# Kernel optimization log

Measured on AMD Instinct MI355X. Metric: run time of the kernel, lower is better.

## Reference

```python
import jax, jax.numpy as jnp
import numpy as np

B = 4096  # number of rows (batch of 1-D sequences)
N = 4096  # transform length


def setup_inputs() -> dict:
    key = jax.random.key(0)
    x = jax.random.normal(key, (B, N), dtype=jnp.float32)
    # get_expk(N): expk[k] = (cos(pi*k/(2N)), -sin(pi*k/(2N)))
    t = jnp.arange(N, dtype=jnp.float32) * (np.pi / (2.0 * N))
    expk = jnp.stack([jnp.cos(t), -jnp.sin(t)], axis=-1)  # [N, 2]
    return {"x": x, "expk": expk}


def reference(x, expk):
    # IDCT (DCT-III), 2N-point FFT formulation:
    #   y_k = x_0 + 2 * sum_{n=1}^{N-1} x_n cos(pi*n*(2k+1)/(2N))
    #       = Re{ sum_n w_n x_n exp(j*pi*n/(2N)) * exp(j*2*pi*n*k/(2N)) },  w_0=1, w_n=2
    # i.e. the first N outputs of a 2N-point inverse DFT of the zero-padded,
    # twiddle-premultiplied sequence.
    n = x.shape[-1]
    # expk stores (cos(theta), -sin(theta)) => exp(+j*theta) = expk0 - j*expk1
    coef = (expk[..., 0] - 1j * expk[..., 1]).astype(jnp.complex64)  # [N]
    w = jnp.concatenate([jnp.ones((1,), x.dtype), jnp.full((n - 1,), 2.0, x.dtype)])
    a = (x * w).astype(jnp.complex64) * coef                      # [B, N]
    A = jnp.concatenate([a, jnp.zeros_like(a)], axis=-1)          # [B, 2N] zero-pad
    y = jnp.real(jnp.fft.ifft(A, axis=-1))[..., :n] * (2.0 * n)   # undo 1/(2N) of ifft
    return y.astype(x.dtype)
```

## Files before the change

### kernel.cpp

```cpp
#include <hip/hip_runtime.h>


#define NROW 4096
#define M    2048
#define NT   128
#define SWZ2(a) ((a) ^ ((((a) >> 4) & 7) << 1))

__device__ __forceinline__ void cmul(float ar, float ai, float br, float bi,
                                     float& orr, float& oii) {
    orr = ar * br - ai * bi;
    oii = ar * bi + ai * br;
}

__device__ __forceinline__ void dft16(float vr[16], float vi[16]) {
    constexpr float WR[4][4] = {
        {1.f, 1.f, 1.f, 1.f},
        {1.f,  0.92387953251128674f,  0.70710678118654752f,  0.38268343236508977f},
        {1.f,  0.70710678118654752f,  0.f,                  -0.70710678118654752f},
        {1.f,  0.38268343236508977f, -0.70710678118654752f, -0.92387953251128674f}};
    constexpr float WI[4][4] = {
        {0.f, 0.f, 0.f, 0.f},
        {0.f,  0.38268343236508977f,  0.70710678118654752f,  0.92387953251128674f},
        {0.f,  0.70710678118654752f,  1.f,                   0.70710678118654752f},
        {0.f,  0.92387953251128674f,  0.70710678118654752f, -0.38268343236508977f}};
    float ur[16], ui[16];
#pragma unroll
    for (int p = 0; p < 4; ++p) {
        float apcr = vr[p] + vr[p + 8],      apci = vi[p] + vi[p + 8];
        float amcr = vr[p] - vr[p + 8],      amci = vi[p] - vi[p + 8];
        float bpdr = vr[p + 4] + vr[p + 12], bpdi = vi[p + 4] + vi[p + 12];
        float bmdr = vr[p + 4] - vr[p + 12], bmdi = vi[p + 4] - vi[p + 12];
        float y0r = apcr + bpdr, y0i = apci + bpdi;
        float y1r = amcr - bmdi, y1i = amci + bmdr;
        float y2r = apcr - bpdr, y2i = apci - bpdi;
        float y3r = amcr + bmdi, y3i = amci - bmdr;
        ur[4 * p + 0] = y0r;  ui[4 * p + 0] = y0i;
        cmul(y1r, y1i, WR[p][1], WI[p][1], ur[4 * p + 1], ui[4 * p + 1]);
        cmul(y2r, y2i, WR[p][2], WI[p][2], ur[4 * p + 2], ui[4 * p + 2]);
        cmul(y3r, y3i, WR[p][3], WI[p][3], ur[4 * p + 3], ui[4 * p + 3]);
    }
#pragma unroll
    for (int q = 0; q < 4; ++q) {
        float apcr = ur[q] + ur[q + 8],      apci = ui[q] + ui[q + 8];
        float amcr = ur[q] - ur[q + 8],      amci = ui[q] - ui[q + 8];
        float bpdr = ur[q + 4] + ur[q + 12], bpdi = ui[q + 4] + ui[q + 12];
        float bmdr = ur[q + 4] - ur[q + 12], bmdi = ui[q + 4] - ui[q + 12];
        vr[q]      = apcr + bpdr;  vi[q]      = apci + bpdi;
        vr[q + 4]  = amcr - bmdi;  vi[q + 4]  = amci + bmdr;
        vr[q + 8]  = apcr - bpdr;  vi[q + 8]  = apci - bpdi;
        vr[q + 12] = amcr + bmdi;  vi[q + 12] = amci - bmdr;
    }
}

__device__ __forceinline__ void dft4(float& ar, float& ai, float& br, float& bi,
                                     float& cr, float& ci, float& dr, float& di) {
    float s02r = ar + cr, s02i = ai + ci;
    float d02r = ar - cr, d02i = ai - ci;
    float s13r = br + dr, s13i = bi + di;
    float d13r = br - dr, d13i = bi - di;
    ar = s02r + s13r; ai = s02i + s13i;
    br = d02r - d13i; bi = d02i + d13r;
    cr = s02r - s13r; ci = s02i - s13i;
    dr = d02r + d13i; di = d02i - d13r;
}

__device__ __forceinline__ void dft8(float* vr, float* vi) {
    float er[4]  = {vr[0], vr[2], vr[4], vr[6]};
    float ei[4]  = {vi[0], vi[2], vi[4], vi[6]};
    float odr[4] = {vr[1], vr[3], vr[5], vr[7]};
    float odi[4] = {vi[1], vi[3], vi[5], vi[7]};
    dft4(er[0], ei[0], er[1], ei[1], er[2], ei[2], er[3], ei[3]);
    dft4(odr[0], odi[0], odr[1], odi[1], odr[2], odi[2], odr[3], odi[3]);
    const float s = 0.70710678118654752f;
    vr[0] = er[0] + odr[0];            vi[0] = ei[0] + odi[0];
    vr[4] = er[0] - odr[0];            vi[4] = ei[0] - odi[0];
    float t1r = s * (odr[1] - odi[1]), t1i = s * (odr[1] + odi[1]);
    vr[1] = er[1] + t1r;               vi[1] = ei[1] + t1i;
    vr[5] = er[1] - t1r;               vi[5] = ei[1] - t1i;
    vr[2] = er[2] - odi[2];            vi[2] = ei[2] + odr[2];
    vr[6] = er[2] + odi[2];            vi[6] = ei[2] - odr[2];
    float t3r = -s * (odr[3] + odi[3]), t3i = s * (odr[3] - odi[3]);
    vr[3] = er[3] + t3r;               vi[3] = ei[3] + t3i;
    vr[7] = er[3] - t3r;               vi[7] = ei[3] - t3i;
}

__device__ __forceinline__ void twiddle_apply(float vr[16], float vi[16],
                                              float w1r, float w1i) {
    float cr = w1r, ci = w1i;
#pragma unroll
    for (int r = 1; r < 16; ++r) {
        float tr, ti;
        cmul(vr[r], vi[r], cr, ci, tr, ti);
        vr[r] = tr; vi[r] = ti;
        if (r < 15) { float nr, ni; cmul(cr, ci, w1r, w1i, nr, ni); cr = nr; ci = ni; }
    }
}

__device__ __forceinline__ void twiddle_apply8(float* vr, float* vi,
                                               float w1r, float w1i) {
    float cr = w1r, ci = w1i;
#pragma unroll
    for (int r = 1; r < 8; ++r) {
        float tr, ti;
        cmul(vr[r], vi[r], cr, ci, tr, ti);
        vr[r] = tr; vi[r] = ti;
        if (r < 7) { float nr, ni; cmul(cr, ci, w1r, w1i, nr, ni); cr = nr; ci = ni; }
    }
}

extern "C" __global__ void __launch_bounds__(NT, 2)
idct_fft_kernel(const float* __restrict__ x, const float* __restrict__ expk,
                float* __restrict__ out)
{
    __shared__ __align__(16) float2 S[M];
    const int tid = threadIdx.x;
    const long row = blockIdx.x;
    const float* __restrict__ xp = x + row * (long)NROW;
    const float2* __restrict__ e2 = (const float2*)expk;

    float vr[16], vi[16];

#pragma unroll
    for (int j = 0; j < 16; ++j) {
        int k = tid + NT * j;
        float x1  = xp[k];
        float x2  = xp[k + M];
        float xr1 = (k == 0) ? 0.0f : xp[NROW - k];
        float xr2 = xp[M - k];
        float2 E1 = e2[k];
        float2 E2 = e2[k + M];
        float c1 = E1.x, s1 = -E1.y;
        float c2 = E2.x, s2 = -E2.y;
        float h1r = c1 * x1 + s1 * xr1, h1i = s1 * x1 - c1 * xr1;
        float h2r = c2 * x2 + s2 * xr2, h2i = s2 * x2 - c2 * xr2;
        int hi = (k >= 1024);
        float2 EW = e2[(4 * k) & (NROW - 1)];
        float wr = hi ? EW.y : EW.x;
        float wi = hi ? EW.x : -EW.y;
        float Sr = h1r + h2r, Si = h1i + h2i;
        float Dr = h1r - h2r, Di = h1i - h2i;
        vr[j] = Sr - (wr * Di + wi * Dr);
        vi[j] = Si + (wr * Dr - wi * Di);
    }
    dft16(vr, vi);
    { float2 E = e2[8 * tid]; twiddle_apply(vr, vi, E.x, -E.y); }
#pragma unroll
    for (int rp = 0; rp < 8; ++rp) {
        int a = 16 * tid + 2 * rp;
        *(float4*)&S[SWZ2(a)] =
            make_float4(vr[2 * rp], vi[2 * rp], vr[2 * rp + 1], vi[2 * rp + 1]);
    }
    __syncthreads();

    const int p2 = tid & 15, t0a = tid >> 4;
#pragma unroll
    for (int h = 0; h < 2; ++h) {
        int t0 = t0a + 8 * h;
#pragma unroll
        for (int t1 = 0; t1 < 8; ++t1) {
            float2 c = S[SWZ2(16 * t0 + 256 * t1 + p2)];
            vr[8 * h + t1] = c.x; vi[8 * h + t1] = c.y;
        }
    }
    __syncthreads();
    dft8(vr, vi);
    dft8(vr + 8, vi + 8);
    { float2 E = e2[128 * t0a];       twiddle_apply8(vr, vi, E.x, -E.y); }
    { float2 E = e2[128 * (t0a + 8)]; twiddle_apply8(vr + 8, vi + 8, E.x, -E.y); }
#pragma unroll
    for (int h = 0; h < 2; ++h) {
        int t0 = t0a + 8 * h;
#pragma unroll
        for (int q0 = 0; q0 < 8; ++q0) {
            S[SWZ2(t0 + 16 * p2 + 256 * q0)] = make_float2(vr[8 * h + q0], vi[8 * h + q0]);
        }
    }
    __syncthreads();

    const int p3 = tid & 15, q03 = tid >> 4;
    {
        int base = 16 * p3 + 256 * q03;
#pragma unroll
        for (int tp = 0; tp < 8; ++tp) {
            float4 c = *(const float4*)&S[SWZ2(base + 2 * tp)];
            vr[2 * tp] = c.x; vi[2 * tp] = c.y; vr[2 * tp + 1] = c.z; vi[2 * tp + 1] = c.w;
        }
    }
    __syncthreads();
    dft16(vr, vi);
#pragma unroll
    for (int q1 = 0; q1 < 16; ++q1) {
        S[SWZ2(tid + 128 * q1)] = make_float2(vr[q1], vi[q1]);
    }
    __syncthreads();

    float4* __restrict__ y4 = (float4*)(out + row * (long)NROW);
#pragma unroll
    for (int v = 0; v < 8; ++v) {
        int u = tid + NT * v;
        float2 zu = S[SWZ2(u)];
        float2 zv = S[SWZ2(M - 1 - u)];
        y4[u] = make_float4(zu.x, zv.y, zu.y, zv.x);
    }
}

extern "C" void kernel_launch(void* const* d_in, const int* in_sizes, int n_in,
                              void* d_out, int out_size, void* d_ws, size_t ws_size,
                              hipStream_t stream) {
    const float* x    = (const float*)d_in[0];
    const float* expk = (const float*)d_in[1];
    float* out        = (float*)d_out;
    const int nrows   = in_sizes[0] / NROW;
    hipLaunchKernelGGL(idct_fft_kernel, dim3(nrows), dim3(NT), 0, stream,
                       x, expk, out);
}
```

Measured before the change: 137.0 us.

## Restructure 2048-point FFT as 8x8x8x4 stages with 256 threads

Replaces the 16x8x16 radix decomposition run by 128 threads with an 8x8x8x4 decomposition run by 256 threads, each holding 8 complex values. Shared memory is double-buffered so some barriers can be dropped. The final radix-4 stage writes output directly from registers using mirrored index pairs, removing the last shared-memory round trip. Occupancy is raised through launch bounds (256, 6) and a lower register footprint, in exchange for an extra FFT stage and more shared-memory passes.

Result: faster. 133.6 us (-2.5%).

```diff
diff --git a/kernel.cpp b/kernel.cpp
--- a/kernel.cpp
+++ b/kernel.cpp
@@ -2,54 +2,14 @@
 
 
 #define NROW 4096
-#define M    2048
-#define NT   128
-#define SWZ2(a) ((a) ^ ((((a) >> 4) & 7) << 1))
+#define MM   2048
+#define NT   256
+#define SWZ(a) ((a) ^ ((((a) >> 6) & 7) << 1))
 
 __device__ __forceinline__ void cmul(float ar, float ai, float br, float bi,
                                      float& orr, float& oii) {
     orr = ar * br - ai * bi;
     oii = ar * bi + ai * br;
-}
-
-__device__ __forceinline__ void dft16(float vr[16], float vi[16]) {
-    constexpr float WR[4][4] = {
-        {1.f, 1.f, 1.f, 1.f},
-        {1.f,  0.92387953251128674f,  0.70710678118654752f,  0.38268343236508977f},
-        {1.f,  0.70710678118654752f,  0.f,                  -0.70710678118654752f},
-        {1.f,  0.38268343236508977f, -0.70710678118654752f, -0.92387953251128674f}};
-    constexpr float WI[4][4] = {
-        {0.f, 0.f, 0.f, 0.f},
-        {0.f,  0.38268343236508977f,  0.70710678118654752f,  0.92387953251128674f},
-        {0.f,  0.70710678118654752f,  1.f,                   0.70710678118654752f},
-        {0.f,  0.92387953251128674f,  0.70710678118654752f, -0.38268343236508977f}};
-    float ur[16], ui[16];
-#pragma unroll
-    for (int p = 0; p < 4; ++p) {
-        float apcr = vr[p] + vr[p + 8],      apci = vi[p] + vi[p + 8];
-        float amcr = vr[p] - vr[p + 8],      amci = vi[p] - vi[p + 8];
-        float bpdr = vr[p + 4] + vr[p + 12], bpdi = vi[p + 4] + vi[p + 12];
-        float bmdr = vr[p + 4] - vr[p + 12], bmdi = vi[p + 4] - vi[p + 12];
-        float y0r = apcr + bpdr, y0i = apci + bpdi;
-        float y1r = amcr - bmdi, y1i = amci + bmdr;
-        float y2r = apcr - bpdr, y2i = apci - bpdi;
-        float y3r = amcr + bmdi, y3i = amci - bmdr;
-        ur[4 * p + 0] = y0r;  ui[4 * p + 0] = y0i;
-        cmul(y1r, y1i, WR[p][1], WI[p][1], ur[4 * p + 1], ui[4 * p + 1]);
-        cmul(y2r, y2i, WR[p][2], WI[p][2], ur[4 * p + 2], ui[4 * p + 2]);
-        cmul(y3r, y3i, WR[p][3], WI[p][3], ur[4 * p + 3], ui[4 * p + 3]);
-    }
-#pragma unroll
-    for (int q = 0; q < 4; ++q) {
-        float apcr = ur[q] + ur[q + 8],      apci = ui[q] + ui[q + 8];
-        float amcr = ur[q] - ur[q + 8],      amci = ui[q] - ui[q + 8];
-        float bpdr = ur[q + 4] + ur[q + 12], bpdi = ui[q + 4] + ui[q + 12];
-        float bmdr = ur[q + 4] - ur[q + 12], bmdi = ui[q + 4] - ui[q + 12];
-        vr[q]      = apcr + bpdr;  vi[q]      = apci + bpdi;
-        vr[q + 4]  = amcr - bmdi;  vi[q + 4]  = amci + bmdr;
-        vr[q + 8]  = apcr - bpdr;  vi[q + 8]  = apci - bpdi;
-        vr[q + 12] = amcr + bmdi;  vi[q + 12] = amci - bmdr;
-    }
 }
 
 __device__ __forceinline__ void dft4(float& ar, float& ai, float& br, float& bi,
@@ -84,20 +44,8 @@
     vr[7] = er[3] - t3r;               vi[7] = ei[3] - t3i;
 }
 
-__device__ __forceinline__ void twiddle_apply(float vr[16], float vi[16],
-                                              float w1r, float w1i) {
-    float cr = w1r, ci = w1i;
-#pragma unroll
-    for (int r = 1; r < 16; ++r) {
-        float tr, ti;
-        cmul(vr[r], vi[r], cr, ci, tr, ti);
-        vr[r] = tr; vi[r] = ti;
-        if (r < 15) { float nr, ni; cmul(cr, ci, w1r, w1i, nr, ni); cr = nr; ci = ni; }
-    }
-}
-
-__device__ __forceinline__ void twiddle_apply8(float* vr, float* vi,
-                                               float w1r, float w1i) {
+__device__ __forceinline__ void twiddle_in8(float* vr, float* vi,
+                                            float w1r, float w1i) {
     float cr = w1r, ci = w1i;
 #pragma unroll
     for (int r = 1; r < 8; ++r) {
@@ -108,27 +56,28 @@
     }
 }
 
-extern "C" __global__ void __launch_bounds__(NT, 2)
+extern "C" __global__ void __launch_bounds__(NT, 6)
 idct_fft_kernel(const float* __restrict__ x, const float* __restrict__ expk,
                 float* __restrict__ out)
 {
-    __shared__ __align__(16) float2 S[M];
+    __shared__ __align__(16) float2 BA[MM];
+    __shared__ __align__(16) float2 BB[MM];
     const int tid = threadIdx.x;
     const long row = blockIdx.x;
     const float* __restrict__ xp = x + row * (long)NROW;
     const float2* __restrict__ e2 = (const float2*)expk;
 
-    float vr[16], vi[16];
+    float vr[8], vi[8];
 
 #pragma unroll
-    for (int j = 0; j < 16; ++j) {
-        int k = tid + NT * j;
+    for (int r = 0; r < 8; ++r) {
+        int k = tid + NT * r;
         float x1  = xp[k];
-        float x2  = xp[k + M];
+        float x2  = xp[k + MM];
         float xr1 = (k == 0) ? 0.0f : xp[NROW - k];
-        float xr2 = xp[M - k];
+        float xr2 = xp[MM - k];
         float2 E1 = e2[k];
-        float2 E2 = e2[k + M];
+        float2 E2 = e2[k + MM];
         float c1 = E1.x, s1 = -E1.y;
         float c2 = E2.x, s2 = -E2.y;
         float h1r = c1 * x1 + s1 * xr1, h1i = s1 * x1 - c1 * xr1;
@@ -139,69 +88,87 @@
         float wi = hi ? EW.x : -EW.y;
         float Sr = h1r + h2r, Si = h1i + h2i;
         float Dr = h1r - h2r, Di = h1i - h2i;
-        vr[j] = Sr - (wr * Di + wi * Dr);
-        vi[j] = Si + (wr * Dr - wi * Di);
+        vr[r] = Sr - (wr * Di + wi * Dr);
+        vi[r] = Si + (wr * Dr - wi * Di);
     }
-    dft16(vr, vi);
-    { float2 E = e2[8 * tid]; twiddle_apply(vr, vi, E.x, -E.y); }
+    dft8(vr, vi);
 #pragma unroll
-    for (int rp = 0; rp < 8; ++rp) {
-        int a = 16 * tid + 2 * rp;
-        *(float4*)&S[SWZ2(a)] =
-            make_float4(vr[2 * rp], vi[2 * rp], vr[2 * rp + 1], vi[2 * rp + 1]);
+    for (int j = 0; j < 4; ++j) {
+        int a = 8 * tid + 2 * j;
+        *(float4*)&BA[SWZ(a)] =
+            make_float4(vr[2 * j], vi[2 * j], vr[2 * j + 1], vi[2 * j + 1]);
     }
     __syncthreads();
 
-    const int p2 = tid & 15, t0a = tid >> 4;
 #pragma unroll
-    for (int h = 0; h < 2; ++h) {
-        int t0 = t0a + 8 * h;
+    for (int r = 0; r < 8; ++r) {
+        float2 c = BA[SWZ(tid + 256 * r)];
+        vr[r] = c.x; vi[r] = c.y;
+    }
+    {
+        float2 E = e2[256 * (tid & 7)];
+        twiddle_in8(vr, vi, E.x, -E.y);
+    }
+    dft8(vr, vi);
+    {
+        int p = tid & 7, t = tid >> 3;
 #pragma unroll
-        for (int t1 = 0; t1 < 8; ++t1) {
-            float2 c = S[SWZ2(16 * t0 + 256 * t1 + p2)];
-            vr[8 * h + t1] = c.x; vi[8 * h + t1] = c.y;
-        }
-    }
-    __syncthreads();
-    dft8(vr, vi);
-    dft8(vr + 8, vi + 8);
-    { float2 E = e2[128 * t0a];       twiddle_apply8(vr, vi, E.x, -E.y); }
-    { float2 E = e2[128 * (t0a + 8)]; twiddle_apply8(vr + 8, vi + 8, E.x, -E.y); }
-#pragma unroll
-    for (int h = 0; h < 2; ++h) {
-        int t0 = t0a + 8 * h;
-#pragma unroll
-        for (int q0 = 0; q0 < 8; ++q0) {
-            S[SWZ2(t0 + 16 * p2 + 256 * q0)] = make_float2(vr[8 * h + q0], vi[8 * h + q0]);
-        }
+        for (int q = 0; q < 8; ++q)
+            BB[SWZ(p + 8 * q + 64 * t)] = make_float2(vr[q], vi[q]);
     }
     __syncthreads();
 
-    const int p3 = tid & 15, q03 = tid >> 4;
+#pragma unroll
+    for (int r = 0; r < 8; ++r) {
+        float2 c = BB[SWZ(tid + 256 * r)];
+        vr[r] = c.x; vi[r] = c.y;
+    }
     {
-        int base = 16 * p3 + 256 * q03;
+        float2 E = e2[32 * (tid & 63)];
+        twiddle_in8(vr, vi, E.x, -E.y);
+    }
+    dft8(vr, vi);
+    {
+        int p = tid & 63, t = tid >> 6;
 #pragma unroll
-        for (int tp = 0; tp < 8; ++tp) {
-            float4 c = *(const float4*)&S[SWZ2(base + 2 * tp)];
-            vr[2 * tp] = c.x; vi[2 * tp] = c.y; vr[2 * tp + 1] = c.z; vi[2 * tp + 1] = c.w;
-        }
-    }
-    __syncthreads();
-    dft16(vr, vi);
-#pragma unroll
-    for (int q1 = 0; q1 < 16; ++q1) {
-        S[SWZ2(tid + 128 * q1)] = make_float2(vr[q1], vi[q1]);
+        for (int q = 0; q < 8; ++q)
+            BA[SWZ(p + 64 * q + 512 * t)] = make_float2(vr[q], vi[q]);
     }
     __syncthreads();
 
+    float ar[4], ai[4], br4[4], bi4[4];
+    const int pB = 511 - tid;
+#pragma unroll
+    for (int r = 0; r < 4; ++r) {
+        float2 cA = BA[SWZ(tid + 512 * r)];
+        ar[r] = cA.x; ai[r] = cA.y;
+        float2 cB = BA[SWZ(pB + 512 * r)];
+        br4[r] = cB.x; bi4[r] = cB.y;
+    }
+    {
+        float2 EA = e2[8 * tid];
+        float wAr = EA.x, wAi = -EA.y, cr = wAr, ci = wAi;
+#pragma unroll
+        for (int r = 1; r < 4; ++r) {
+            float tr, ti; cmul(ar[r], ai[r], cr, ci, tr, ti); ar[r] = tr; ai[r] = ti;
+            if (r < 3) { float nr, ni; cmul(cr, ci, wAr, wAi, nr, ni); cr = nr; ci = ni; }
+        }
+        float2 EB = e2[8 * pB];
+        float wBr = EB.x, wBi = -EB.y; cr = wBr; ci = wBi;
+#pragma unroll
+        for (int r = 1; r < 4; ++r) {
+            float tr, ti; cmul(br4[r], bi4[r], cr, ci, tr, ti); br4[r] = tr; bi4[r] = ti;
+            if (r < 3) { float nr, ni; cmul(cr, ci, wBr, wBi, nr, ni); cr = nr; ci = ni; }
+        }
+    }
+    dft4(ar[0], ai[0], ar[1], ai[1], ar[2], ai[2], ar[3], ai[3]);
+    dft4(br4[0], bi4[0], br4[1], bi4[1], br4[2], bi4[2], br4[3], bi4[3]);
+
     float4* __restrict__ y4 = (float4*)(out + row * (long)NROW);
-#pragma unroll
-    for (int v = 0; v < 8; ++v) {
-        int u = tid + NT * v;
-        float2 zu = S[SWZ2(u)];
-        float2 zv = S[SWZ2(M - 1 - u)];
-        y4[u] = make_float4(zu.x, zv.y, zu.y, zv.x);
-    }
+    y4[tid]        = make_float4(ar[0],  bi4[3], ai[0],  br4[3]);
+    y4[tid + 512]  = make_float4(ar[1],  bi4[2], ai[1],  br4[2]);
+    y4[1023 - tid] = make_float4(br4[1], ai[2],  bi4[1], ar[2]);
+    y4[511 - tid]  = make_float4(br4[0], ai[3],  bi4[0], ar[3]);
 }
 
 extern "C" void kernel_launch(void* const* d_in, const int* in_sizes, int n_in,
```
